# Kernel optimization log

Hardware: AMD Instinct MI355X
Metric: run time of the kernel (lower is better)

The kernel has to match this reference:

```python
import jax, jax.numpy as jnp
import numpy as np

N = 10000        # nodes
E = 160000       # edges (avg degree 16)
IN = 8 * 144     # 1152
OUT = 2 * 144    # 288 per ChebConv
KS = [4, 5, 6, 7]


def setup_inputs() -> dict:
    key = jax.random.key(0)
    ks = jax.random.split(key, 10)
    x = jax.random.normal(ks[0], (N, IN), dtype=jnp.float32)
    edge_index = jax.random.randint(ks[1], (2, E), 0, N, dtype=jnp.int32)
    d = {"x": x, "edge_index": edge_index}
    for i, (name, K) in enumerate(zip(["3", "5", "7", "9"], KS)):
        d["W" + name] = jax.random.normal(ks[2 + i], (K, IN, OUT), dtype=jnp.float32) * 0.02
        d["b" + name] = jnp.zeros((OUT,), dtype=jnp.float32)
    return d


def _cheb_basis(x, edge_index, K):
    """Chebyshev basis T_0..T_{K-1} of L_hat = -D^{-1/2} A D^{-1/2} (lambda_max=2,
    as in PyG ChebConv default; self-loop term 2/lambda_max - 1 = 0)."""
    row, col = edge_index[0], edge_index[1]  # source, target
    n = x.shape[0]
    w = jnp.ones(row.shape, x.dtype)
    deg = jax.ops.segment_sum(w, row, num_segments=n)
    dinv = jnp.where(deg > 0, jax.lax.rsqrt(jnp.maximum(deg, 1e-12)), 0.0)
    norm = -(dinv[row] * dinv[col])  # [E]

    def prop(h):  # out[i] = sum_{j->i} norm_e * h[j]
        return jax.ops.segment_sum(h[row] * norm[:, None], col, num_segments=n)

    Tx = [x, prop(x)]
    for _ in range(K - 2):
        Tx.append(2.0 * prop(Tx[-1]) - Tx[-2])
    return jnp.stack(Tx[:K], axis=0)  # [K, N, F]


def reference(x, edge_index, W3, b3, W5, b5, W7, b7, W9, b9):
    T = _cheb_basis(x, edge_index, max(KS))  # shared basis; identical math per conv
    outs = []
    for W, b in ((W3, b3), (W5, b5), (W7, b7), (W9, b9)):
        K = W.shape[0]
        outs.append(jnp.einsum('knf,kfo->no', T[:K], W) + b)
    return jnp.concatenate(outs, axis=1)  # [N, 4*OUT]
```

## Files before the change

kernel.cpp:

```cpp
#include <hip/hip_runtime.h>

#define NN 10000
#define NE 160000
#define FIN 1152
#define FOUT 288
#define FOUT_TOTAL 1152
#define NF (NN * FOUT)
#define WSL (FIN * FOUT)
#define NSLICE 22
#define NMT 79
#define GEMM_BLOCKS 5688

typedef __attribute__((ext_vector_type(8))) short short8;
typedef __attribute__((ext_vector_type(8))) unsigned short ushort8v;
typedef __attribute__((ext_vector_type(4))) float floatx4;

__device__ __forceinline__ unsigned short f2bf(float f) {
  unsigned int u = __float_as_uint(f);
  u += 0x7FFF + ((u >> 16) & 1);
  return (unsigned short)(u >> 16);
}
__device__ __forceinline__ float bf2f(unsigned short u) {
  return __uint_as_float(((unsigned int)u) << 16);
}

__device__ __forceinline__ void async_copy16(void* lds, const void* gmem) {
  __builtin_amdgcn_global_load_lds(
      (const __attribute__((address_space(1))) unsigned int*)gmem,
      (__attribute__((address_space(3))) unsigned int*)lds, 16, 0, 0);
}


__global__ void deg_kernel(const int* __restrict__ ei, int* __restrict__ deg,
                           int* __restrict__ indeg) {
  int e = blockIdx.x * 256 + threadIdx.x;
  if (e < NE) {
    atomicAdd(&deg[ei[e]], 1);
    atomicAdd(&indeg[ei[NE + e]], 1);
  }
}

__global__ void dinv_kernel(const int* __restrict__ deg, float* __restrict__ dinv) {
  int i = blockIdx.x * 256 + threadIdx.x;
  if (i < NN) {
    int d = deg[i];
    dinv[i] = d > 0 ? rsqrtf((float)d) : 0.0f;
  }
}

__global__ __launch_bounds__(256) void scan_kernel(
    const int* __restrict__ indeg, int* __restrict__ rowptr,
    int* __restrict__ cursor) {
  __shared__ int buf[10240];
  __shared__ int sums[256];
  const int t = threadIdx.x;
  for (int i = t; i < 10240; i += 256) buf[i] = (i < NN) ? indeg[i] : 0;
  __syncthreads();
  const int base = t * 40;
  int tot = 0;
#pragma unroll
  for (int j = 0; j < 40; j++) tot += buf[base + j];
  sums[t] = tot;
  __syncthreads();
  for (int off = 1; off < 256; off <<= 1) {
    int v = (t >= off) ? sums[t - off] : 0;
    __syncthreads();
    sums[t] += v;
    __syncthreads();
  }
  int run = sums[t] - tot;
#pragma unroll
  for (int j = 0; j < 40; j++) {
    int v = buf[base + j];
    buf[base + j] = run;
    run += v;
  }
  __syncthreads();
  for (int i = t; i < NN; i += 256) {
    int v = buf[i];
    rowptr[i] = v;
    cursor[i] = v;
  }
  if (t == 255) rowptr[NN] = sums[255];
}

__global__ void scatter_kernel(const int* __restrict__ ei, const float* __restrict__ dinv,
                               int* __restrict__ cursor, int* __restrict__ srcarr,
                               float* __restrict__ wn) {
  int e = blockIdx.x * 256 + threadIdx.x;
  if (e < NE) {
    int r = ei[e], c = ei[NE + e];
    int pos = atomicAdd(&cursor[c], 1);
    srcarr[pos] = r;
    wn[pos] = -(dinv[r] * dinv[c]);
  }
}

__global__ __launch_bounds__(256) void wtrans_kernel(
    const float* __restrict__ W0, const float* __restrict__ W1,
    const float* __restrict__ W2, const float* __restrict__ W3,
    unsigned short* __restrict__ Wt) {
  __shared__ float tile[32][33];
  const int s = blockIdx.y;
  int c, k;
  if (s < 4)       { c = 0; k = s; }
  else if (s < 9)  { c = 1; k = s - 4; }
  else if (s < 15) { c = 2; k = s - 9; }
  else             { c = 3; k = s - 15; }
  const float* W = ((c == 0) ? W0 : (c == 1) ? W1 : (c == 2) ? W2 : W3) +
                   (size_t)k * WSL;
  const int bx = blockIdx.x;
  const int f0 = (bx % 36) * 32;
  const int o0 = (bx / 36) * 32;
  const int tx = threadIdx.x & 31;
  const int ty = threadIdx.x >> 5;
#pragma unroll
  for (int jj = 0; jj < 4; jj++)
    tile[ty + 8 * jj][tx] = W[(size_t)(f0 + ty + 8 * jj) * FOUT + (o0 + tx)];
  __syncthreads();
  unsigned short* dst = Wt + (size_t)s * WSL;
#pragma unroll
  for (int jj = 0; jj < 4; jj++)
    dst[(size_t)(o0 + ty + 8 * jj) * FIN + (f0 + tx)] = f2bf(tile[tx][ty + 8 * jj]);
}

__global__ void xcast_kernel(const float* __restrict__ x, unsigned short* __restrict__ xb) {
  int i = blockIdx.x * 256 + threadIdx.x;
  if (i < NN * FIN / 4) {
    float4 v = *(const float4*)(x + (size_t)i * 4);
    ushort4 r;
    r.x = f2bf(v.x); r.y = f2bf(v.y); r.z = f2bf(v.z); r.w = f2bf(v.w);
    *(ushort4*)(xb + (size_t)i * 4) = r;
  }
}

__global__ __launch_bounds__(256) void gemm_mfma_kernel(
    const unsigned short* __restrict__ Xb, const unsigned short* __restrict__ Wt,
    unsigned short* __restrict__ Yall) {
  const int L = blockIdx.x;
  const int j = L & 7;
  const int m = L >> 3;
  const int nsl = (j < 6) ? 3 : 2;
  const int work = nsl * 3 * NMT;
  if (m >= work) return;
  const int mtile = m / (nsl * 3);
  const int rem = m - mtile * (nsl * 3);
  const int slice = j + 8 * (rem / 3);
  const int n0 = (rem % 3) * 96;
  const int m0 = mtile * 128;

  __shared__ unsigned short As[128][64];
  __shared__ unsigned short Bs[96][64];

  const int tid = threadIdx.x;
  const int lane = tid & 63;
  const int wave = tid >> 6;
  const int wx = wave & 1;
  const int wy = wave >> 1;
  const int lm = lane & 15;
  const int hi = lane >> 4;

  floatx4 acc[4][3];
#pragma unroll
  for (int i = 0; i < 4; i++)
#pragma unroll
    for (int jj = 0; jj < 3; jj++) acc[i][jj] = (floatx4){0.f, 0.f, 0.f, 0.f};

  const unsigned short* Wbase = Wt + (size_t)slice * WSL;

  for (int f0 = 0; f0 < FIN; f0 += 64) {
    __syncthreads();
#pragma unroll
    for (int i = 0; i < 4; i++) {
      int idx = i * 256 + tid;
      int row = idx >> 3;
      int ck = idx & 7;
      int gr = m0 + row;
      gr = gr < NN ? gr : NN - 1;
      async_copy16((char*)&As[0][0] + idx * 16,
                   (const char*)Xb + ((size_t)gr * FIN + f0) * 2 + ((ck ^ (row & 7)) << 4));
    }
#pragma unroll
    for (int i = 0; i < 3; i++) {
      int idx = i * 256 + tid;
      int row = idx >> 3;
      int ck = idx & 7;
      async_copy16((char*)&Bs[0][0] + idx * 16,
                   (const char*)Wbase + ((size_t)(n0 + row) * FIN + f0) * 2 + ((ck ^ (row & 7)) << 4));
    }
    __syncthreads();
#pragma unroll
    for (int s = 0; s < 2; s++) {
      short8 a[4], b[3];
#pragma unroll
      for (int i = 0; i < 4; i++) {
        int ar = wy * 64 + i * 16 + lm;
        a[i] = *(const short8*)((const char*)&As[ar][0] + (((s * 4 + hi) ^ (ar & 7)) << 4));
      }
#pragma unroll
      for (int jj = 0; jj < 3; jj++) {
        int br = wx * 48 + jj * 16 + lm;
        b[jj] = *(const short8*)((const char*)&Bs[br][0] + (((s * 4 + hi) ^ (br & 7)) << 4));
      }
#pragma unroll
      for (int i = 0; i < 4; i++)
#pragma unroll
        for (int jj = 0; jj < 3; jj++)
          acc[i][jj] = __builtin_amdgcn_mfma_f32_16x16x32_bf16(a[i], b[jj], acc[i][jj], 0, 0, 0);
    }
  }
  unsigned short* Yb = Yall + (size_t)slice * NF;
  const int cbase = n0 + wx * 48 + lm;
  const int rbase = (lane >> 4) * 4;
#pragma unroll
  for (int i = 0; i < 4; i++) {
#pragma unroll
    for (int r = 0; r < 4; r++) {
      int grow = m0 + wy * 64 + i * 16 + rbase + r;
      if (grow < NN) {
        unsigned short* op = Yb + (size_t)grow * FOUT + cbase;
#pragma unroll
        for (int jj = 0; jj < 3; jj++) op[jj * 16] = f2bf(acc[i][jj][r]);
      }
    }
  }
}


struct StepA {
  const unsigned short* H[4];
  const unsigned short* Y[4];
  const unsigned short* P[4];
  unsigned short* D[4];
};

template <int NACT>
__global__ __launch_bounds__(576) void cl_step_fused(
    StepA a, const int* __restrict__ rowptr, const int* __restrict__ srcarr,
    const float* __restrict__ wn) {
  const int t = threadIdx.x;
  const int nodesub = t / 72;
  const int rem = t - nodesub * 72;
  const int ln = rem >> 1;
  const int half = rem & 1;
  const int node = blockIdx.x * 8 + nodesub;
  const int off = ln * 8;
  const int rs0 = rowptr[node];
  const int re0 = rowptr[node + 1];
  const int mid = rs0 + ((re0 - rs0 + 1) >> 1);
  const int rs = half ? mid : rs0;
  const int re = half ? re0 : mid;
  float acc[NACT][8];
#pragma unroll
  for (int s = 0; s < NACT; s++)
#pragma unroll
    for (int q = 0; q < 8; q++) acc[s][q] = 0.f;

  constexpr int U = (NACT <= 2) ? 4 : 2;
  int p = rs;
  for (; p + U <= re; p += U) {
    int r[U];
    float w[U];
#pragma unroll
    for (int u = 0; u < U; u++) { r[u] = srcarr[p + u]; w[u] = wn[p + u]; }
    ushort8v h[U][NACT];
#pragma unroll
    for (int u = 0; u < U; u++)
#pragma unroll
      for (int s = 0; s < NACT; s++)
        h[u][s] = *(const ushort8v*)(a.H[s] + (size_t)r[u] * FOUT + off);
#pragma unroll
    for (int u = 0; u < U; u++)
#pragma unroll
      for (int s = 0; s < NACT; s++)
#pragma unroll
        for (int q = 0; q < 8; q++) acc[s][q] += w[u] * bf2f(h[u][s][q]);
  }
  for (; p < re; ++p) {
    int r = srcarr[p];
    float w = wn[p];
#pragma unroll
    for (int s = 0; s < NACT; s++) {
      ushort8v hh = *(const ushort8v*)(a.H[s] + (size_t)r * FOUT + off);
#pragma unroll
      for (int q = 0; q < 8; q++) acc[s][q] += w * bf2f(hh[q]);
    }
  }

#pragma unroll
  for (int s = 0; s < NACT; s++)
#pragma unroll
    for (int q = 0; q < 8; q++) acc[s][q] += __shfl_xor(acc[s][q], 1, 64);

  if (half == 0) {
    size_t o = (size_t)node * FOUT + off;
#pragma unroll
    for (int s = 0; s < NACT; s++) {
      ushort8v y = *(const ushort8v*)(a.Y[s] + o);
      ushort8v d;
      if (a.P[s]) {
        ushort8v pp = *(const ushort8v*)(a.P[s] + o);
#pragma unroll
        for (int q = 0; q < 8; q++)
          d[q] = f2bf(bf2f(y[q]) + 2.f * acc[s][q] - bf2f(pp[q]));
      } else {
#pragma unroll
        for (int q = 0; q < 8; q++) d[q] = f2bf(bf2f(y[q]) + 2.f * acc[s][q]);
      }
      *(ushort8v*)(a.D[s] + o) = d;
    }
  }
}

struct FinalA {
  const unsigned short* H[4];
  const unsigned short* Y[4];
  const unsigned short* P[4];
  const float* B[4];
  int conv[4];
};

__global__ __launch_bounds__(576) void cl_final_fused(
    FinalA a, const int* __restrict__ rowptr, const int* __restrict__ srcarr,
    const float* __restrict__ wn, float* __restrict__ out) {
  const int t = threadIdx.x;
  const int nodesub = t / 72;
  const int rem = t - nodesub * 72;
  const int ln = rem >> 1;
  const int half = rem & 1;
  const int node = blockIdx.x * 8 + nodesub;
  const int off = ln * 8;
  const int rs0 = rowptr[node];
  const int re0 = rowptr[node + 1];
  const int mid = rs0 + ((re0 - rs0 + 1) >> 1);
  const int rs = half ? mid : rs0;
  const int re = half ? re0 : mid;
  float acc[4][8];
#pragma unroll
  for (int s = 0; s < 4; s++)
#pragma unroll
    for (int q = 0; q < 8; q++) acc[s][q] = 0.f;

  constexpr int U = 2;
  int p = rs;
  for (; p + U <= re; p += U) {
    int r[U];
    float w[U];
#pragma unroll
    for (int u = 0; u < U; u++) { r[u] = srcarr[p + u]; w[u] = wn[p + u]; }
    ushort8v h[U][4];
#pragma unroll
    for (int u = 0; u < U; u++)
#pragma unroll
      for (int s = 0; s < 4; s++)
        h[u][s] = *(const ushort8v*)(a.H[s] + (size_t)r[u] * FOUT + off);
#pragma unroll
    for (int u = 0; u < U; u++)
#pragma unroll
      for (int s = 0; s < 4; s++)
#pragma unroll
        for (int q = 0; q < 8; q++) acc[s][q] += w[u] * bf2f(h[u][s][q]);
  }
  for (; p < re; ++p) {
    int r = srcarr[p];
    float w = wn[p];
#pragma unroll
    for (int s = 0; s < 4; s++) {
      ushort8v hh = *(const ushort8v*)(a.H[s] + (size_t)r * FOUT + off);
#pragma unroll
      for (int q = 0; q < 8; q++) acc[s][q] += w * bf2f(hh[q]);
    }
  }

#pragma unroll
  for (int s = 0; s < 4; s++)
#pragma unroll
    for (int q = 0; q < 8; q++) acc[s][q] += __shfl_xor(acc[s][q], 1, 64);

  if (half == 0) {
    size_t o = (size_t)node * FOUT + off;
#pragma unroll
    for (int s = 0; s < 4; s++) {
      ushort8v y = *(const ushort8v*)(a.Y[s] + o);
      ushort8v pp = *(const ushort8v*)(a.P[s] + o);
      const float* bias = a.B[s] + off;
      float r8[8];
#pragma unroll
      for (int q = 0; q < 8; q++)
        r8[q] = bias[q] + bf2f(y[q]) + acc[s][q] - bf2f(pp[q]);
      float* op = out + (size_t)node * FOUT_TOTAL + a.conv[s] * FOUT + off;
      *(float4*)(op + 0) = make_float4(r8[0], r8[1], r8[2], r8[3]);
      *(float4*)(op + 4) = make_float4(r8[4], r8[5], r8[6], r8[7]);
    }
  }
}


extern "C" void kernel_launch(void* const* d_in, const int* in_sizes, int n_in,
                              void* d_out, int out_size, void* d_ws, size_t ws_size,
                              hipStream_t stream) {
  const float* x = (const float*)d_in[0];
  const int* ei = (const int*)d_in[1];
  const float* W[4] = {(const float*)d_in[2], (const float*)d_in[4],
                       (const float*)d_in[6], (const float*)d_in[8]};
  const float* b[4] = {(const float*)d_in[3], (const float*)d_in[5],
                       (const float*)d_in[7], (const float*)d_in[9]};
  float* out = (float*)d_out;

  char* ws = (char*)d_ws;
  size_t off = 0;
  auto alloc = [&](size_t bytes) -> char* {
    char* p = ws + off;
    off += (bytes + 255) & ~(size_t)255;
    return p;
  };
  int* deg = (int*)alloc(NN * 4);
  int* indeg = (int*)alloc(NN * 4);
  int* rowptr = (int*)alloc((NN + 1) * 4);
  int* cursor = (int*)alloc(NN * 4);
  int* srcarr = (int*)alloc(NE * 4);
  float* wn = (float*)alloc(NE * 4);
  float* dinv = (float*)alloc(NN * 4);
  unsigned short* xb = (unsigned short*)alloc((size_t)NN * FIN * 2);
  unsigned short* Wt = (unsigned short*)alloc((size_t)NSLICE * WSL * 2);
  unsigned short* Yall = (unsigned short*)alloc((size_t)NSLICE * NF * 2);

  hipMemsetAsync(deg, 0, NN * 4, stream);
  hipMemsetAsync(indeg, 0, NN * 4, stream);

  deg_kernel<<<(NE + 255) / 256, 256, 0, stream>>>(ei, deg, indeg);
  dinv_kernel<<<(NN + 255) / 256, 256, 0, stream>>>(deg, dinv);
  scan_kernel<<<1, 256, 0, stream>>>(indeg, rowptr, cursor);
  scatter_kernel<<<(NE + 255) / 256, 256, 0, stream>>>(ei, dinv, cursor, srcarr, wn);
  wtrans_kernel<<<dim3(324, NSLICE), 256, 0, stream>>>(W[0], W[1], W[2], W[3], Wt);
  xcast_kernel<<<(NN * FIN / 4 + 255) / 256, 256, 0, stream>>>(x, xb);

  gemm_mfma_kernel<<<GEMM_BLOCKS, 256, 0, stream>>>(xb, Wt, Yall);

  const int nK[4] = {4, 5, 6, 7};
  const int st[4] = {0, 4, 9, 15};
  unsigned short* S[4];
  for (int c = 0; c < 4; c++) S[c] = xb + (size_t)c * NF;

  StepA sched[5];
  int nact[5] = {0, 0, 0, 0, 0};
  FinalA fa;

  for (int c = 3; c >= 0; c--) {
    int n = nK[c] - 1;
    int s0 = 6 - n;
    unsigned short* Yn = Yall + (size_t)(st[c] + n) * NF;
    unsigned short* A = S[c];
    for (int p = 1; p <= n; p++) {
      int s = s0 + p - 1;
      if (p < n) {
        unsigned short* H = (p & 1) ? Yn : A;
        unsigned short* D = (p & 1) ? A : Yn;
        int j = nact[s]++;
        sched[s].H[j] = H;
        sched[s].Y[j] = Yall + (size_t)(st[c] + n - p) * NF;
        sched[s].P[j] = (p == 1) ? nullptr : D;
        sched[s].D[j] = D;
      } else {
        int j = 3 - c;
        fa.H[j] = ((n - 1) & 1) ? A : Yn;
        fa.P[j] = ((n - 2) & 1) ? A : Yn;
        fa.Y[j] = Yall + (size_t)st[c] * NF;
        fa.B[j] = b[c];
        fa.conv[j] = c;
      }
    }
  }

  for (int s = 0; s < 5; s++)
    for (int j = nact[s]; j < 4; j++) {
      sched[s].H[j] = sched[s].H[0];
      sched[s].Y[j] = sched[s].Y[0];
      sched[s].P[j] = sched[s].P[0];
      sched[s].D[j] = sched[s].D[0];
    }

  const int grid_cl = NN / 8;
  for (int s = 0; s < 5; s++) {
    switch (nact[s]) {
      case 1: cl_step_fused<1><<<grid_cl, 576, 0, stream>>>(sched[s], rowptr, srcarr, wn); break;
      case 2: cl_step_fused<2><<<grid_cl, 576, 0, stream>>>(sched[s], rowptr, srcarr, wn); break;
      case 3: cl_step_fused<3><<<grid_cl, 576, 0, stream>>>(sched[s], rowptr, srcarr, wn); break;
      default: cl_step_fused<4><<<grid_cl, 576, 0, stream>>>(sched[s], rowptr, srcarr, wn); break;
    }
  }
  cl_final_fused<<<grid_cl, 576, 0, stream>>>(fa, rowptr, srcarr, wn, out);
}
```

Baseline: 657.1 us.

## Split SpMM feature columns into 8 jobs per 32-node block

Reworks the propagation kernels so each block covers 32 nodes and one eighth of the feature columns (36 features), with 18 threads per node each handling 4 bf16 values instead of 8. Blocks with the same node group but different column jobs are adjacent, which aims to improve L2 locality of the gathered neighbor rows and to raise parallelism and reduce per-thread register pressure. In exchange, loads become 8-byte instead of 16-byte, and edge indices and weights are re-read by 8 times as many threads.

```diff
diff --git a/kernel.cpp b/kernel.cpp
--- a/kernel.cpp
+++ b/kernel.cpp
@@ -13,6 +13,7 @@
 
 typedef __attribute__((ext_vector_type(8))) short short8;
 typedef __attribute__((ext_vector_type(8))) unsigned short ushort8v;
+typedef __attribute__((ext_vector_type(4))) unsigned short ushort4v;
 typedef __attribute__((ext_vector_type(4))) float floatx4;
 
 __device__ __forceinline__ unsigned short f2bf(float f) {
@@ -238,23 +239,26 @@
 __global__ __launch_bounds__(576) void cl_step_fused(
     StepA a, const int* __restrict__ rowptr, const int* __restrict__ srcarr,
     const float* __restrict__ wn) {
+  const int job = blockIdx.x & 7;
+  const int nb = blockIdx.x >> 3;
   const int t = threadIdx.x;
-  const int nodesub = t / 72;
-  const int rem = t - nodesub * 72;
+  const int nl = t / 18;
+  const int rem = t - nl * 18;
   const int ln = rem >> 1;
   const int half = rem & 1;
-  const int node = blockIdx.x * 8 + nodesub;
-  const int off = ln * 8;
+  const int node = nb * 32 + nl;
+  if (node >= NN) return;
+  const int off = (job * 9 + ln) * 4;
   const int rs0 = rowptr[node];
   const int re0 = rowptr[node + 1];
   const int mid = rs0 + ((re0 - rs0 + 1) >> 1);
   const int rs = half ? mid : rs0;
   const int re = half ? re0 : mid;
-  float acc[NACT][8];
+  float acc[NACT][4];
 #pragma unroll
   for (int s = 0; s < NACT; s++)
 #pragma unroll
-    for (int q = 0; q < 8; q++) acc[s][q] = 0.f;
+    for (int q = 0; q < 4; q++) acc[s][q] = 0.f;
 
   constexpr int U = (NACT <= 2) ? 4 : 2;
   int p = rs;
@@ -263,51 +267,51 @@
     float w[U];
 #pragma unroll
     for (int u = 0; u < U; u++) { r[u] = srcarr[p + u]; w[u] = wn[p + u]; }
-    ushort8v h[U][NACT];
+    ushort4v h[U][NACT];
 #pragma unroll
     for (int u = 0; u < U; u++)
 #pragma unroll
       for (int s = 0; s < NACT; s++)
-        h[u][s] = *(const ushort8v*)(a.H[s] + (size_t)r[u] * FOUT + off);
+        h[u][s] = *(const ushort4v*)(a.H[s] + (size_t)r[u] * FOUT + off);
 #pragma unroll
     for (int u = 0; u < U; u++)
 #pragma unroll
       for (int s = 0; s < NACT; s++)
 #pragma unroll
-        for (int q = 0; q < 8; q++) acc[s][q] += w[u] * bf2f(h[u][s][q]);
+        for (int q = 0; q < 4; q++) acc[s][q] += w[u] * bf2f(h[u][s][q]);
   }
   for (; p < re; ++p) {
     int r = srcarr[p];
     float w = wn[p];
 #pragma unroll
     for (int s = 0; s < NACT; s++) {
-      ushort8v hh = *(const ushort8v*)(a.H[s] + (size_t)r * FOUT + off);
-#pragma unroll
-      for (int q = 0; q < 8; q++) acc[s][q] += w * bf2f(hh[q]);
+      ushort4v hh = *(const ushort4v*)(a.H[s] + (size_t)r * FOUT + off);
+#pragma unroll
+      for (int q = 0; q < 4; q++) acc[s][q] += w * bf2f(hh[q]);
     }
   }
 
 #pragma unroll
   for (int s = 0; s < NACT; s++)
 #pragma unroll
-    for (int q = 0; q < 8; q++) acc[s][q] += __shfl_xor(acc[s][q], 1, 64);
+    for (int q = 0; q < 4; q++) acc[s][q] += __shfl_xor(acc[s][q], 1, 64);
 
   if (half == 0) {
     size_t o = (size_t)node * FOUT + off;
 #pragma unroll
     for (int s = 0; s < NACT; s++) {
-      ushort8v y = *(const ushort8v*)(a.Y[s] + o);
-      ushort8v d;
+      ushort4v y = *(const ushort4v*)(a.Y[s] + o);
+      ushort4v d;
       if (a.P[s]) {
-        ushort8v pp = *(const ushort8v*)(a.P[s] + o);
-#pragma unroll
-        for (int q = 0; q < 8; q++)
+        ushort4v pp = *(const ushort4v*)(a.P[s] + o);
+#pragma unroll
+        for (int q = 0; q < 4; q++)
           d[q] = f2bf(bf2f(y[q]) + 2.f * acc[s][q] - bf2f(pp[q]));
       } else {
 #pragma unroll
-        for (int q = 0; q < 8; q++) d[q] = f2bf(bf2f(y[q]) + 2.f * acc[s][q]);
+        for (int q = 0; q < 4; q++) d[q] = f2bf(bf2f(y[q]) + 2.f * acc[s][q]);
       }
-      *(ushort8v*)(a.D[s] + o) = d;
+      *(ushort4v*)(a.D[s] + o) = d;
     }
   }
 }
@@ -323,23 +327,26 @@
 __global__ __launch_bounds__(576) void cl_final_fused(
     FinalA a, const int* __restrict__ rowptr, const int* __restrict__ srcarr,
     const float* __restrict__ wn, float* __restrict__ out) {
+  const int job = blockIdx.x & 7;
+  const int nb = blockIdx.x >> 3;
   const int t = threadIdx.x;
-  const int nodesub = t / 72;
-  const int rem = t - nodesub * 72;
+  const int nl = t / 18;
+  const int rem = t - nl * 18;
   const int ln = rem >> 1;
   const int half = rem & 1;
-  const int node = blockIdx.x * 8 + nodesub;
-  const int off = ln * 8;
+  const int node = nb * 32 + nl;
+  if (node >= NN) return;
+  const int off = (job * 9 + ln) * 4;
   const int rs0 = rowptr[node];
   const int re0 = rowptr[node + 1];
   const int mid = rs0 + ((re0 - rs0 + 1) >> 1);
   const int rs = half ? mid : rs0;
   const int re = half ? re0 : mid;
-  float acc[4][8];
+  float acc[4][4];
 #pragma unroll
   for (int s = 0; s < 4; s++)
 #pragma unroll
-    for (int q = 0; q < 8; q++) acc[s][q] = 0.f;
+    for (int q = 0; q < 4; q++) acc[s][q] = 0.f;
 
   constexpr int U = 2;
   int p = rs;
@@ -348,49 +355,48 @@
     float w[U];
 #pragma unroll
     for (int u = 0; u < U; u++) { r[u] = srcarr[p + u]; w[u] = wn[p + u]; }
-    ushort8v h[U][4];
+    ushort4v h[U][4];
 #pragma unroll
     for (int u = 0; u < U; u++)
 #pragma unroll
       for (int s = 0; s < 4; s++)
-        h[u][s] = *(const ushort8v*)(a.H[s] + (size_t)r[u] * FOUT + off);
+        h[u][s] = *(const ushort4v*)(a.H[s] + (size_t)r[u] * FOUT + off);
 #pragma unroll
     for (int u = 0; u < U; u++)
 #pragma unroll
       for (int s = 0; s < 4; s++)
 #pragma unroll
-        for (int q = 0; q < 8; q++) acc[s][q] += w[u] * bf2f(h[u][s][q]);
+        for (int q = 0; q < 4; q++) acc[s][q] += w[u] * bf2f(h[u][s][q]);
   }
   for (; p < re; ++p) {
     int r = srcarr[p];
     float w = wn[p];
 #pragma unroll
     for (int s = 0; s < 4; s++) {
-      ushort8v hh = *(const ushort8v*)(a.H[s] + (size_t)r * FOUT + off);
-#pragma unroll
-      for (int q = 0; q < 8; q++) acc[s][q] += w * bf2f(hh[q]);
+      ushort4v hh = *(const ushort4v*)(a.H[s] + (size_t)r * FOUT + off);
+#pragma unroll
+      for (int q = 0; q < 4; q++) acc[s][q] += w * bf2f(hh[q]);
     }
   }
 
 #pragma unroll
   for (int s = 0; s < 4; s++)
 #pragma unroll
-    for (int q = 0; q < 8; q++) acc[s][q] += __shfl_xor(acc[s][q], 1, 64);
+    for (int q = 0; q < 4; q++) acc[s][q] += __shfl_xor(acc[s][q], 1, 64);
 
   if (half == 0) {
     size_t o = (size_t)node * FOUT + off;
 #pragma unroll
     for (int s = 0; s < 4; s++) {
-      ushort8v y = *(const ushort8v*)(a.Y[s] + o);
-      ushort8v pp = *(const ushort8v*)(a.P[s] + o);
+      ushort4v y = *(const ushort4v*)(a.Y[s] + o);
+      ushort4v pp = *(const ushort4v*)(a.P[s] + o);
       const float* bias = a.B[s] + off;
-      float r8[8];
-#pragma unroll
-      for (int q = 0; q < 8; q++)
-        r8[q] = bias[q] + bf2f(y[q]) + acc[s][q] - bf2f(pp[q]);
+      float r4[4];
+#pragma unroll
+      for (int q = 0; q < 4; q++)
+        r4[q] = bias[q] + bf2f(y[q]) + acc[s][q] - bf2f(pp[q]);
       float* op = out + (size_t)node * FOUT_TOTAL + a.conv[s] * FOUT + off;
-      *(float4*)(op + 0) = make_float4(r8[0], r8[1], r8[2], r8[3]);
-      *(float4*)(op + 4) = make_float4(r8[4], r8[5], r8[6], r8[7]);
+      *(float4*)op = make_float4(r4[0], r4[1], r4[2], r4[3]);
     }
   }
 }
@@ -480,7 +486,7 @@
       sched[s].D[j] = sched[s].D[0];
     }
 
-  const int grid_cl = NN / 8;
+  const int grid_cl = 8 * ((NN + 31) / 32);
   for (int s = 0; s < 5; s++) {
     switch (nact[s]) {
       case 1: cl_step_fused<1><<<grid_cl, 576, 0, stream>>>(sched[s], rowptr, srcarr, wn); break;
```

Measured after the change: 836.1 us. 27.2% more time.
